# Kernel optimization log

Measured on AMD Instinct MI355X. Metric: run time of the kernel, lower is better.

## Reference

```python
import jax, jax.numpy as jnp
import numpy as np

N = 100000        # nodes
E = 1600000       # edges (before self-loops)
IN_CH = 256       # input features
HEADS = 8         # conv1 heads; per-head dim also 8 (GATConv(in, heads, heads=heads))
HID = 8
NCLASS = 64
SLOPE = 0.2       # PyG leaky_relu negative slope


def _gat_conv(x, edge_index, W, att_src, att_dst, bias, heads, ch, concat):
    """PyG GATConv (eval mode): gather -> leaky_relu score -> segment softmax -> scatter."""
    n = x.shape[0]
    src, dst = edge_index[0], edge_index[1]
    h = (x @ W).reshape(n, heads, ch)                      # [N, H, C]
    a_src = jnp.einsum('nhc,hc->nh', h, att_src)           # [N, H]
    a_dst = jnp.einsum('nhc,hc->nh', h, att_dst)
    alpha = jax.nn.leaky_relu(a_src[src] + a_dst[dst], SLOPE)  # [E, H]
    # segment softmax over destination node
    amax = jax.ops.segment_max(alpha, dst, num_segments=n)     # [N, H]
    ex = jnp.exp(alpha - amax[dst])
    denom = jax.ops.segment_sum(ex, dst, num_segments=n)
    coef = ex / (denom[dst] + 1e-16)                           # [E, H]
    out = jax.ops.segment_sum(coef[:, :, None] * h[src], dst, num_segments=n)  # [N, H, C]
    if concat:
        out = out.reshape(n, heads * ch)
    else:
        out = out.mean(axis=1)
    return out + bias


def _add_self_loops(edge_index, n):
    loop = jnp.arange(n, dtype=edge_index.dtype)
    return jnp.concatenate([edge_index, jnp.stack([loop, loop])], axis=1)


def setup_inputs() -> dict:
    key = jax.random.key(0)
    ks = jax.random.split(key, 10)
    g = lambda k, shp, s: (jax.random.normal(k, shp, jnp.float32) * s)
    return {
        'x': jax.random.normal(ks[0], (N, IN_CH), jnp.float32),
        'edge_index': jax.random.randint(ks[1], (2, E), 0, N, dtype=jnp.int64),
        'W1': g(ks[2], (IN_CH, HEADS * HID), 1.0 / np.sqrt(IN_CH)),
        'att_src1': g(ks[3], (HEADS, HID), 0.3),
        'att_dst1': g(ks[4], (HEADS, HID), 0.3),
        'b1': jnp.zeros((HEADS * HID,), jnp.float32),
        'W2': g(ks[5], (HEADS * HID, NCLASS), 1.0 / np.sqrt(HEADS * HID)),
        'att_src2': g(ks[6], (1, NCLASS), 0.3),
        'att_dst2': g(ks[7], (1, NCLASS), 0.3),
        'b2': jnp.zeros((NCLASS,), jnp.float32),
    }


def reference(x, edge_index, W1, att_src1, att_dst1, b1, W2, att_src2, att_dst2, b2):
    ei = _add_self_loops(edge_index, x.shape[0])
    h = jax.nn.elu(_gat_conv(x, ei, W1, att_src1, att_dst1, b1, HEADS, HID, True))
    # dropout is a no-op in eval mode
    h = _gat_conv(h, ei, W2, att_src2, att_dst2, b2, 1, NCLASS, False)
    return jax.nn.log_softmax(h, axis=-1)
```

## Files before the change

kernel.cpp:

```cpp
#include <hip/hip_runtime.h>
#include <hip/hip_bf16.h>

#define LRELU_SLOPE 0.2f
#define NBUK 256
#define BCAP 9728
#define CH2 6144

typedef unsigned int uint;
typedef unsigned short ushort;
typedef short bt8 __attribute__((ext_vector_type(8)));
typedef float fx4 __attribute__((ext_vector_type(4)));

__device__ __forceinline__ ushort f2bf(float f) {
    uint u = __float_as_uint(f);
    return (ushort)((u + 0x7FFF + ((u >> 16) & 1)) >> 16);
}
__device__ __forceinline__ float bf2f(ushort h) {
    return __uint_as_float(((uint)h) << 16);
}

#define ACC8(e, hv) \
    acc[0] += (e) * bf2f((ushort)((hv).x & 0xffff)); \
    acc[1] += (e) * bf2f((ushort)((hv).x >> 16));    \
    acc[2] += (e) * bf2f((ushort)((hv).y & 0xffff)); \
    acc[3] += (e) * bf2f((ushort)((hv).y >> 16));    \
    acc[4] += (e) * bf2f((ushort)((hv).z & 0xffff)); \
    acc[5] += (e) * bf2f((ushort)((hv).z >> 16));    \
    acc[6] += (e) * bf2f((ushort)((hv).w & 0xffff)); \
    acc[7] += (e) * bf2f((ushort)((hv).w >> 16));

__global__ __launch_bounds__(256) void prep_init(
    const float* __restrict__ W1, const float* __restrict__ W2,
    ushort* __restrict__ WT1, ushort* __restrict__ WT2, int* __restrict__ pcur)
{
    int t = threadIdx.x;
    int idx = blockIdx.x * 256 + t;
    if (blockIdx.x == 0) pcur[t] = t * BCAP;
    if (idx < 64 * 256) {
        int c = idx >> 8, k = idx & 255;
        WT1[idx] = f2bf(W1[k * 64 + c]);
    }
    int i2 = idx - 64 * 256;
    if (i2 >= 0 && i2 < 64 * 64) {
        int c = i2 >> 6, k = i2 & 63;
        WT2[i2] = f2bf(W2[k * 64 + c]);
    }
}

__global__ __launch_bounds__(1024) void partition_pairs(
    const int* __restrict__ ei, int E_, int ET,
    int* __restrict__ pcur, uint* __restrict__ pairs)
{
    __shared__ int lcnt[NBUK], lsc[NBUK], lplace[NBUK], gpos[NBUK];
    const int t = threadIdx.x;
    const int base = blockIdx.x * CH2;
    const int total = min(CH2, ET - base);
    if (total <= 0) return;

    if (t < NBUK) lcnt[t] = 0;
    __syncthreads();

    uint pp[6]; int pk[6];
    #pragma unroll
    for (int i = 0; i < 6; ++i) {
        int idx = t + i * 1024;
        pk[i] = -1;
        if (idx < total) {
            int e = base + idx;
            int s, d;
            if (e < E_) { s = ei[e]; d = ei[E_ + e]; } else { s = d = e - E_; }
            pk[i] = d >> 9;
            pp[i] = (uint)s | ((uint)(d & 511) << 17);
            atomicAdd(&lcnt[pk[i]], 1);
        }
    }
    __syncthreads();

    if (t < NBUK) lsc[t] = lcnt[t];
    __syncthreads();
    for (int off = 1; off < NBUK; off <<= 1) {
        int add = 0;
        if (t < NBUK && t >= off) add = lsc[t - off];
        __syncthreads();
        if (t < NBUK) lsc[t] += add;
        __syncthreads();
    }
    if (t < NBUK) {
        int excl = lsc[t] - lcnt[t];
        lplace[t] = excl;
        int c = lcnt[t];
        gpos[t] = c ? (atomicAdd(&pcur[t], c) - excl) : 0;
    }
    __syncthreads();

    #pragma unroll
    for (int i = 0; i < 6; ++i) {
        if (pk[i] >= 0) {
            int slot = atomicAdd(&lplace[pk[i]], 1);
            pairs[gpos[pk[i]] + slot] = pp[i];
        }
    }
}

__global__ __launch_bounds__(1024) void phase2_build(
    const uint* __restrict__ pairs, const int* __restrict__ pcur,
    int* __restrict__ rp, int* __restrict__ ssrc, int n, int nbuk_used)
{
    __shared__ int hist[512], cur[512], psc[NBUK];
    const int k = blockIdx.x;
    const int t = threadIdx.x;
    const int beg = k * BCAP;
    const int cnt = pcur[k] - beg;
    const int dbase = k << 9;

    if (t < 512) hist[t] = 0;
    if (t < NBUK) psc[t] = (t < nbuk_used) ? (pcur[t] - t * BCAP) : 0;
    __syncthreads();
    for (int off = 1; off < NBUK; off <<= 1) {
        int add = (t < NBUK && t >= off) ? psc[t - off] : 0;
        __syncthreads();
        if (t < NBUK) psc[t] += add;
        __syncthreads();
    }
    const int bbase = k ? psc[k - 1] : 0;

    for (int i = t; i < cnt; i += 1024)
        atomicAdd(&hist[pairs[beg + i] >> 17], 1);
    __syncthreads();

    int c0 = (t < 512) ? hist[t] : 0;
    for (int off = 1; off < 512; off <<= 1) {
        int add = (t < 512 && t >= off) ? hist[t - off] : 0;
        __syncthreads();
        if (t < 512) hist[t] += add;
        __syncthreads();
    }
    if (t < 512) {
        int node = dbase + t;
        if (node < n) rp[node] = bbase + hist[t];
        cur[t] = hist[t] - c0;
    }
    __syncthreads();

    for (int i = t; i < cnt; i += 1024) {
        uint p = pairs[beg + i];
        int j = p >> 17;
        int pos = bbase + atomicAdd(&cur[j], 1);
        ssrc[pos] = (int)(p & 0x1FFFF);
    }
}

template<int K, bool INF32, int HEADS>
__global__ __launch_bounds__(256) void gemm_att(
    const void* __restrict__ Xv, const ushort* __restrict__ WT,
    ushort* __restrict__ OUT, float* __restrict__ a_src, float* __restrict__ a_dst,
    const float* __restrict__ att_s, const float* __restrict__ att_d, int nrows)
{
    constexpr int LDW = K + 8;
    constexpr int NIT = K / 32;
    __shared__ ushort wt_l[64 * LDW];
    __shared__ ushort a_l[64 * 40];
    const int t = threadIdx.x;
    const int base = blockIdx.x * 64;

    for (int idx = t * 8; idx < 64 * K; idx += 256 * 8) {
        int r = idx / K, c = idx % K;
        *(uint4*)&wt_l[r * LDW + c] = *(const uint4*)&WT[idx];
    }

    const int w = t >> 6, l = t & 63;
    const int frow = l & 15;
    const int kof = (l >> 4) * 8;
    fx4 acc[4] = {};

    float4 rv0, rv1;
    uint4  rb;

    auto load_tile = [&](int k0) {
        if constexpr (INF32) {
            const float* X = (const float*)Xv;
            int kq = (t & 7) * 4;
            int r0 = (t >> 3), r1 = r0 + 32;
            int g0 = base + r0, g1 = base + r1;
            rv0 = make_float4(0.f, 0.f, 0.f, 0.f);
            rv1 = make_float4(0.f, 0.f, 0.f, 0.f);
            if (g0 < nrows) rv0 = *(const float4*)(X + (size_t)g0 * K + k0 + kq);
            if (g1 < nrows) rv1 = *(const float4*)(X + (size_t)g1 * K + k0 + kq);
        } else {
            const ushort* X = (const ushort*)Xv;
            int r = t >> 2, kq = (t & 3) * 8;
            int gr = base + r;
            rb = make_uint4(0, 0, 0, 0);
            if (gr < nrows) rb = *(const uint4*)(X + (size_t)gr * K + k0 + kq);
        }
    };
    auto store_tile = [&]() {
        if constexpr (INF32) {
            int kq = (t & 7) * 4;
            int r0 = (t >> 3);
            ushort4 o0, o1;
            o0.x = f2bf(rv0.x); o0.y = f2bf(rv0.y); o0.z = f2bf(rv0.z); o0.w = f2bf(rv0.w);
            o1.x = f2bf(rv1.x); o1.y = f2bf(rv1.y); o1.z = f2bf(rv1.z); o1.w = f2bf(rv1.w);
            *(ushort4*)&a_l[r0 * 40 + kq] = o0;
            *(ushort4*)&a_l[(r0 + 32) * 40 + kq] = o1;
        } else {
            int r = t >> 2, kq = (t & 3) * 8;
            *(uint4*)&a_l[r * 40 + kq] = rb;
        }
    };

    load_tile(0);
    store_tile();
    for (int it = 0; it < NIT; ++it) {
        if (it + 1 < NIT) load_tile((it + 1) * 32);
        __syncthreads();
        bt8 af = *(const bt8*)&a_l[(16 * w + frow) * 40 + kof];
        #pragma unroll
        for (int g = 0; g < 4; ++g) {
            bt8 bf = *(const bt8*)&wt_l[(16 * g + frow) * LDW + it * 32 + kof];
            acc[g] = __builtin_amdgcn_mfma_f32_16x16x32_bf16(af, bf, acc[g], 0, 0, 0);
        }
        __syncthreads();
        if (it + 1 < NIT) store_tile();
    }

    const int orow0 = base + 16 * w + (l >> 4) * 4;
    const int ocol = l & 15;
    #pragma unroll
    for (int g = 0; g < 4; ++g) {
        #pragma unroll
        for (int r4 = 0; r4 < 4; ++r4) {
            int gr = orow0 + r4;
            if (gr < nrows) OUT[(size_t)gr * 64 + 16 * g + ocol] = f2bf(acc[g][r4]);
        }
    }

    float as_c[4], ad_c[4];
    #pragma unroll
    for (int g = 0; g < 4; ++g) {
        as_c[g] = att_s[16 * g + ocol];
        ad_c[g] = att_d[16 * g + ocol];
    }
    if constexpr (HEADS == 8) {
        #pragma unroll
        for (int r4 = 0; r4 < 4; ++r4) {
            int gr = orow0 + r4;
            #pragma unroll
            for (int g = 0; g < 4; ++g) {
                float ps = acc[g][r4] * as_c[g];
                float pd = acc[g][r4] * ad_c[g];
                ps += __shfl_xor(ps, 1, 64); pd += __shfl_xor(pd, 1, 64);
                ps += __shfl_xor(ps, 2, 64); pd += __shfl_xor(pd, 2, 64);
                ps += __shfl_xor(ps, 4, 64); pd += __shfl_xor(pd, 4, 64);
                if ((l & 7) == 0 && gr < nrows) {
                    int head = 2 * g + ((l >> 3) & 1);
                    a_src[(size_t)gr * 8 + head] = ps;
                    a_dst[(size_t)gr * 8 + head] = pd;
                }
            }
        }
    } else {
        #pragma unroll
        for (int r4 = 0; r4 < 4; ++r4) {
            int gr = orow0 + r4;
            float ps = 0.f, pd = 0.f;
            #pragma unroll
            for (int g = 0; g < 4; ++g) {
                ps += acc[g][r4] * as_c[g];
                pd += acc[g][r4] * ad_c[g];
            }
            ps += __shfl_xor(ps, 1, 64); pd += __shfl_xor(pd, 1, 64);
            ps += __shfl_xor(ps, 2, 64); pd += __shfl_xor(pd, 2, 64);
            ps += __shfl_xor(ps, 4, 64); pd += __shfl_xor(pd, 4, 64);
            ps += __shfl_xor(ps, 8, 64); pd += __shfl_xor(pd, 8, 64);
            if ((l & 15) == 0 && gr < nrows) {
                a_src[gr] = ps;
                a_dst[gr] = pd;
            }
        }
    }
}

__global__ __launch_bounds__(256) void gather_h8(
    const int* __restrict__ rp, const int* __restrict__ ssrc,
    const float* __restrict__ a_src, const float* __restrict__ a_dst,
    const ushort* __restrict__ HB, const float* __restrict__ bias,
    ushort* __restrict__ HACT, int n)
{
    int node = blockIdx.x * 32 + (threadIdx.x >> 3);
    if (node >= n) return;
    int ol = threadIdx.x & 7;
    int end = rp[node];
    int start = node ? rp[node - 1] : 0;
    float adh = a_dst[(size_t)node * 8 + ol];
    float acc[8] = {};
    float dsum = 0.f;

    int i0 = start;
    for (; i0 + 16 <= end; i0 += 16) {
        int svA = ssrc[i0 + ol];
        int svB = ssrc[i0 + 8 + ol];
        #pragma unroll
        for (int j = 0; j < 8; ++j) {
            int sjA = __shfl(svA, j, 8);
            float aA = a_src[(size_t)sjA * 8 + ol] + adh;
            aA = aA > 0.f ? aA : LRELU_SLOPE * aA;
            float eA = __expf(aA);
            uint4 hvA = *(const uint4*)(HB + (size_t)sjA * 64 + ol * 8);
            dsum += eA; ACC8(eA, hvA);
            int sjB = __shfl(svB, j, 8);
            float aB = a_src[(size_t)sjB * 8 + ol] + adh;
            aB = aB > 0.f ? aB : LRELU_SLOPE * aB;
            float eB = __expf(aB);
            uint4 hvB = *(const uint4*)(HB + (size_t)sjB * 64 + ol * 8);
            dsum += eB; ACC8(eB, hvB);
        }
    }
    for (; i0 < end; i0 += 8) {
        int cnt = min(8, end - i0);
        int sv = (ol < cnt) ? ssrc[i0 + ol] : 0;
        #pragma unroll
        for (int j = 0; j < 8; ++j) {
            int sj = __shfl(sv, j, 8);
            float a = a_src[(size_t)sj * 8 + ol] + adh;
            a = a > 0.f ? a : LRELU_SLOPE * a;
            float e = __expf(a);
            e = (j < cnt) ? e : 0.f;
            uint4 hv = *(const uint4*)(HB + (size_t)sj * 64 + ol * 8);
            dsum += e; ACC8(e, hv);
        }
    }
    float inv = 1.f / (dsum + 1e-16f);
    float4 b0 = *(const float4*)(bias + ol * 8);
    float4 b1 = *(const float4*)(bias + ol * 8 + 4);
    float v[8];
    v[0] = acc[0] * inv + b0.x; v[1] = acc[1] * inv + b0.y;
    v[2] = acc[2] * inv + b0.z; v[3] = acc[3] * inv + b0.w;
    v[4] = acc[4] * inv + b1.x; v[5] = acc[5] * inv + b1.y;
    v[6] = acc[6] * inv + b1.z; v[7] = acc[7] * inv + b1.w;
    #pragma unroll
    for (int c = 0; c < 8; ++c) v[c] = v[c] > 0.f ? v[c] : expm1f(v[c]);
    uint4 o;
    o.x = (uint)f2bf(v[0]) | ((uint)f2bf(v[1]) << 16);
    o.y = (uint)f2bf(v[2]) | ((uint)f2bf(v[3]) << 16);
    o.z = (uint)f2bf(v[4]) | ((uint)f2bf(v[5]) << 16);
    o.w = (uint)f2bf(v[6]) | ((uint)f2bf(v[7]) << 16);
    *(uint4*)(HACT + (size_t)node * 64 + ol * 8) = o;
}

__global__ __launch_bounds__(256) void gather_h1_lsm(
    const int* __restrict__ rp, const int* __restrict__ ssrc,
    const float* __restrict__ a_src, const float* __restrict__ a_dst,
    const ushort* __restrict__ HB, const float* __restrict__ bias,
    float* __restrict__ OUT, int n)
{
    int node = blockIdx.x * 32 + (threadIdx.x >> 3);
    if (node >= n) return;
    int ol = threadIdx.x & 7;
    int end = rp[node];
    int start = node ? rp[node - 1] : 0;
    float ad = a_dst[node];
    float acc[8] = {};
    float dsum = 0.f;

    int i0 = start;
    for (; i0 + 16 <= end; i0 += 16) {
        int svA = ssrc[i0 + ol];
        int svB = ssrc[i0 + 8 + ol];
        #pragma unroll
        for (int j = 0; j < 8; ++j) {
            int sjA = __shfl(svA, j, 8);
            float aA = a_src[sjA] + ad;
            aA = aA > 0.f ? aA : LRELU_SLOPE * aA;
            float eA = __expf(aA);
            uint4 hvA = *(const uint4*)(HB + (size_t)sjA * 64 + ol * 8);
            dsum += eA; ACC8(eA, hvA);
            int sjB = __shfl(svB, j, 8);
            float aB = a_src[sjB] + ad;
            aB = aB > 0.f ? aB : LRELU_SLOPE * aB;
            float eB = __expf(aB);
            uint4 hvB = *(const uint4*)(HB + (size_t)sjB * 64 + ol * 8);
            dsum += eB; ACC8(eB, hvB);
        }
    }
    for (; i0 < end; i0 += 8) {
        int cnt = min(8, end - i0);
        int sv = (ol < cnt) ? ssrc[i0 + ol] : 0;
        #pragma unroll
        for (int j = 0; j < 8; ++j) {
            int sj = __shfl(sv, j, 8);
            float a = a_src[sj] + ad;
            a = a > 0.f ? a : LRELU_SLOPE * a;
            float e = __expf(a);
            e = (j < cnt) ? e : 0.f;
            uint4 hv = *(const uint4*)(HB + (size_t)sj * 64 + ol * 8);
            dsum += e; ACC8(e, hv);
        }
    }
    float inv = 1.f / (dsum + 1e-16f);
    float4 b0 = *(const float4*)(bias + ol * 8);
    float4 b1 = *(const float4*)(bias + ol * 8 + 4);
    float v[8];
    v[0] = acc[0] * inv + b0.x; v[1] = acc[1] * inv + b0.y;
    v[2] = acc[2] * inv + b0.z; v[3] = acc[3] * inv + b0.w;
    v[4] = acc[4] * inv + b1.x; v[5] = acc[5] * inv + b1.y;
    v[6] = acc[6] * inv + b1.z; v[7] = acc[7] * inv + b1.w;

    float m = v[0];
    #pragma unroll
    for (int c = 1; c < 8; ++c) m = fmaxf(m, v[c]);
    m = fmaxf(m, __shfl_xor(m, 1, 8));
    m = fmaxf(m, __shfl_xor(m, 2, 8));
    m = fmaxf(m, __shfl_xor(m, 4, 8));
    float s = 0.f;
    #pragma unroll
    for (int c = 0; c < 8; ++c) s += __expf(v[c] - m);
    s += __shfl_xor(s, 1, 8);
    s += __shfl_xor(s, 2, 8);
    s += __shfl_xor(s, 4, 8);
    float lse = m + __logf(s);
    float4 o0 = make_float4(v[0] - lse, v[1] - lse, v[2] - lse, v[3] - lse);
    float4 o1 = make_float4(v[4] - lse, v[5] - lse, v[6] - lse, v[7] - lse);
    *(float4*)(OUT + (size_t)node * 64 + ol * 8) = o0;
    *(float4*)(OUT + (size_t)node * 64 + ol * 8 + 4) = o1;
}

extern "C" void kernel_launch(void* const* d_in, const int* in_sizes, int n_in,
                              void* d_out, int out_size, void* d_ws, size_t ws_size,
                              hipStream_t stream)
{
    const float* x    = (const float*)d_in[0];
    const int*   ei   = (const int*)d_in[1];
    const float* W1   = (const float*)d_in[2];
    const float* as1w = (const float*)d_in[3];
    const float* ad1w = (const float*)d_in[4];
    const float* b1   = (const float*)d_in[5];
    const float* W2   = (const float*)d_in[6];
    const float* as2w = (const float*)d_in[7];
    const float* ad2w = (const float*)d_in[8];
    const float* b2   = (const float*)d_in[9];
    float* out = (float*)d_out;

    const int n  = in_sizes[0] / 256;
    const int E_ = in_sizes[1] / 2;
    const int ET = E_ + n;
    const int NBUKU = (n + 511) >> 9;

    char* wsb = (char*)d_ws;
    uint*   pairs= (uint*)wsb;
    ushort* HB   = (ushort*)(pairs + (size_t)NBUK*BCAP);
    ushort* HACT = HB + (size_t)n * 64;
    float*  a_s1 = (float*)(HACT + (size_t)n * 64);
    float*  a_d1 = a_s1 + (size_t)n * 8;
    float*  a_s2 = a_d1 + (size_t)n * 8;
    float*  a_d2 = a_s2 + n;
    int*    rp   = (int*)(a_d2 + n);
    int*    pcur = rp + n;
    int*    ssrc = pcur + NBUK;
    ushort* WT1  = (ushort*)(ssrc + ET);
    ushort* WT2  = WT1 + 64 * 256;

    const int gemm_grid = (n + 63) / 64;
    const int gath_grid = (n + 31) / 32;
    const int part_grid = (ET + CH2 - 1) / CH2;

    prep_init<<<80, 256, 0, stream>>>(W1, W2, WT1, WT2, pcur);
    partition_pairs<<<part_grid, 1024, 0, stream>>>(ei, E_, ET, pcur, pairs);
    phase2_build<<<NBUKU, 1024, 0, stream>>>(pairs, pcur, rp, ssrc, n, NBUKU);
    gemm_att<256, true, 8><<<gemm_grid, 256, 0, stream>>>(
        x, WT1, HB, a_s1, a_d1, as1w, ad1w, n);
    gather_h8<<<gath_grid, 256, 0, stream>>>(rp, ssrc, a_s1, a_d1, HB, b1, HACT, n);
    gemm_att<64, false, 1><<<gemm_grid, 256, 0, stream>>>(
        HACT, WT2, HB, a_s2, a_d2, as2w, ad2w, n);
    gather_h1_lsm<<<gath_grid, 256, 0, stream>>>(rp, ssrc, a_s2, a_d2, HB, b2, out, n);
}
```

Measured before the change: 190.0 us.

## Fuse edge partition and layer-1 GEMM into one heterogeneous kernel launch

```diff
diff --git a/kernel.cpp b/kernel.cpp
--- a/kernel.cpp
+++ b/kernel.cpp
@@ -47,13 +47,13 @@
     }
 }
 
-__global__ __launch_bounds__(1024) void partition_pairs(
-    const int* __restrict__ ei, int E_, int ET,
-    int* __restrict__ pcur, uint* __restrict__ pairs)
-{
-    __shared__ int lcnt[NBUK], lsc[NBUK], lplace[NBUK], gpos[NBUK];
+__device__ __forceinline__ void partition_body(
+    int bid, const int* __restrict__ ei, int E_, int ET,
+    int* __restrict__ pcur, uint* __restrict__ pairs,
+    int* lcnt, int* lsc, int* lplace, int* gpos)
+{
     const int t = threadIdx.x;
-    const int base = blockIdx.x * CH2;
+    const int base = bid * CH2;
     const int total = min(CH2, ET - base);
     if (total <= 0) return;
 
@@ -102,6 +102,115 @@
     }
 }
 
+__device__ __forceinline__ void gemm1_body4(
+    int gbid, const float* __restrict__ X, const ushort* __restrict__ WT,
+    ushort* __restrict__ OUT, float* __restrict__ a_src, float* __restrict__ a_dst,
+    const float* __restrict__ att_s, const float* __restrict__ att_d, int nrows,
+    ushort* wt_l, ushort* a_l)
+{
+    constexpr int K = 256, LDW = K + 8, NIT = K / 32;
+    const int t = threadIdx.x;
+    const int tt = t & 255;
+    const int base = (gbid * 4 + (t >> 8)) * 64;
+
+    for (int idx = t * 8; idx < 64 * K; idx += 1024 * 8) {
+        int r = idx / K, c = idx % K;
+        *(uint4*)&wt_l[r * LDW + c] = *(const uint4*)&WT[idx];
+    }
+
+    const int w = tt >> 6, l = tt & 63;
+    const int frow = l & 15;
+    const int kof = (l >> 4) * 8;
+    fx4 acc[4] = {};
+    float4 rv0, rv1;
+
+    auto load_tile = [&](int k0) {
+        int kq = (tt & 7) * 4;
+        int r0 = (tt >> 3);
+        int g0 = base + r0, g1 = base + r0 + 32;
+        rv0 = make_float4(0.f, 0.f, 0.f, 0.f);
+        rv1 = make_float4(0.f, 0.f, 0.f, 0.f);
+        if (g0 < nrows) rv0 = *(const float4*)(X + (size_t)g0 * K + k0 + kq);
+        if (g1 < nrows) rv1 = *(const float4*)(X + (size_t)g1 * K + k0 + kq);
+    };
+    auto store_tile = [&]() {
+        int kq = (tt & 7) * 4;
+        int r0 = (tt >> 3);
+        ushort4 o0, o1;
+        o0.x = f2bf(rv0.x); o0.y = f2bf(rv0.y); o0.z = f2bf(rv0.z); o0.w = f2bf(rv0.w);
+        o1.x = f2bf(rv1.x); o1.y = f2bf(rv1.y); o1.z = f2bf(rv1.z); o1.w = f2bf(rv1.w);
+        *(ushort4*)&a_l[r0 * 40 + kq] = o0;
+        *(ushort4*)&a_l[(r0 + 32) * 40 + kq] = o1;
+    };
+
+    load_tile(0);
+    store_tile();
+    for (int it = 0; it < NIT; ++it) {
+        if (it + 1 < NIT) load_tile((it + 1) * 32);
+        __syncthreads();
+        bt8 af = *(const bt8*)&a_l[(16 * w + frow) * 40 + kof];
+        #pragma unroll
+        for (int g = 0; g < 4; ++g) {
+            bt8 bf = *(const bt8*)&wt_l[(16 * g + frow) * LDW + it * 32 + kof];
+            acc[g] = __builtin_amdgcn_mfma_f32_16x16x32_bf16(af, bf, acc[g], 0, 0, 0);
+        }
+        __syncthreads();
+        if (it + 1 < NIT) store_tile();
+    }
+
+    const int orow0 = base + 16 * w + (l >> 4) * 4;
+    const int ocol = l & 15;
+    #pragma unroll
+    for (int g = 0; g < 4; ++g) {
+        #pragma unroll
+        for (int r4 = 0; r4 < 4; ++r4) {
+            int gr = orow0 + r4;
+            if (gr < nrows) OUT[(size_t)gr * 64 + 16 * g + ocol] = f2bf(acc[g][r4]);
+        }
+    }
+
+    float as_c[4], ad_c[4];
+    #pragma unroll
+    for (int g = 0; g < 4; ++g) {
+        as_c[g] = att_s[16 * g + ocol];
+        ad_c[g] = att_d[16 * g + ocol];
+    }
+    #pragma unroll
+    for (int r4 = 0; r4 < 4; ++r4) {
+        int gr = orow0 + r4;
+        #pragma unroll
+        for (int g = 0; g < 4; ++g) {
+            float ps = acc[g][r4] * as_c[g];
+            float pd = acc[g][r4] * ad_c[g];
+            ps += __shfl_xor(ps, 1, 64); pd += __shfl_xor(pd, 1, 64);
+            ps += __shfl_xor(ps, 2, 64); pd += __shfl_xor(pd, 2, 64);
+            ps += __shfl_xor(ps, 4, 64); pd += __shfl_xor(pd, 4, 64);
+            if ((l & 7) == 0 && gr < nrows) {
+                int head = 2 * g + ((l >> 3) & 1);
+                a_src[(size_t)gr * 8 + head] = ps;
+                a_dst[(size_t)gr * 8 + head] = pd;
+            }
+        }
+    }
+}
+
+__global__ __launch_bounds__(1024) void part_gemm1(
+    const int* __restrict__ ei, int E_, int ET, int part_grid,
+    int* __restrict__ pcur, uint* __restrict__ pairs,
+    const float* __restrict__ x, const ushort* __restrict__ WT1,
+    ushort* __restrict__ HB, float* __restrict__ a_s1, float* __restrict__ a_d1,
+    const float* __restrict__ att_s, const float* __restrict__ att_d, int n)
+{
+    __shared__ int lcnt[NBUK], lsc[NBUK], lplace[NBUK], gpos[NBUK];
+    __shared__ ushort wt_l[64 * 264];
+    __shared__ ushort a_l4[4][64 * 40];
+    if ((int)blockIdx.x < part_grid)
+        partition_body(blockIdx.x, ei, E_, ET, pcur, pairs, lcnt, lsc, lplace, gpos);
+    else
+        gemm1_body4(blockIdx.x - part_grid, x, WT1, HB, a_s1, a_d1,
+                    att_s, att_d, n, wt_l, a_l4[threadIdx.x >> 8]);
+}
+
 __global__ __launch_bounds__(1024) void phase2_build(
     const uint* __restrict__ pairs, const int* __restrict__ pcur,
     int* __restrict__ rp, int* __restrict__ ssrc, int n, int nbuk_used)
@@ -150,14 +259,12 @@
     }
 }
 
-template<int K, bool INF32, int HEADS>
-__global__ __launch_bounds__(256) void gemm_att(
-    const void* __restrict__ Xv, const ushort* __restrict__ WT,
+__global__ __launch_bounds__(256) void gemm2_att(
+    const ushort* __restrict__ X, const ushort* __restrict__ WT,
     ushort* __restrict__ OUT, float* __restrict__ a_src, float* __restrict__ a_dst,
     const float* __restrict__ att_s, const float* __restrict__ att_d, int nrows)
 {
-    constexpr int LDW = K + 8;
-    constexpr int NIT = K / 32;
+    constexpr int K = 64, LDW = K + 8, NIT = K / 32;
     __shared__ ushort wt_l[64 * LDW];
     __shared__ ushort a_l[64 * 40];
     const int t = threadIdx.x;
@@ -172,41 +279,17 @@
     const int frow = l & 15;
     const int kof = (l >> 4) * 8;
     fx4 acc[4] = {};
-
-    float4 rv0, rv1;
-    uint4  rb;
+    uint4 rb;
 
     auto load_tile = [&](int k0) {
-        if constexpr (INF32) {
-            const float* X = (const float*)Xv;
-            int kq = (t & 7) * 4;
-            int r0 = (t >> 3), r1 = r0 + 32;
-            int g0 = base + r0, g1 = base + r1;
-            rv0 = make_float4(0.f, 0.f, 0.f, 0.f);
-            rv1 = make_float4(0.f, 0.f, 0.f, 0.f);
-            if (g0 < nrows) rv0 = *(const float4*)(X + (size_t)g0 * K + k0 + kq);
-            if (g1 < nrows) rv1 = *(const float4*)(X + (size_t)g1 * K + k0 + kq);
-        } else {
-            const ushort* X = (const ushort*)Xv;
-            int r = t >> 2, kq = (t & 3) * 8;
-            int gr = base + r;
-            rb = make_uint4(0, 0, 0, 0);
-            if (gr < nrows) rb = *(const uint4*)(X + (size_t)gr * K + k0 + kq);
-        }
+        int r = t >> 2, kq = (t & 3) * 8;
+        int gr = base + r;
+        rb = make_uint4(0, 0, 0, 0);
+        if (gr < nrows) rb = *(const uint4*)(X + (size_t)gr * K + k0 + kq);
     };
     auto store_tile = [&]() {
-        if constexpr (INF32) {
-            int kq = (t & 7) * 4;
-            int r0 = (t >> 3);
-            ushort4 o0, o1;
-            o0.x = f2bf(rv0.x); o0.y = f2bf(rv0.y); o0.z = f2bf(rv0.z); o0.w = f2bf(rv0.w);
-            o1.x = f2bf(rv1.x); o1.y = f2bf(rv1.y); o1.z = f2bf(rv1.z); o1.w = f2bf(rv1.w);
-            *(ushort4*)&a_l[r0 * 40 + kq] = o0;
-            *(ushort4*)&a_l[(r0 + 32) * 40 + kq] = o1;
-        } else {
-            int r = t >> 2, kq = (t & 3) * 8;
-            *(uint4*)&a_l[r * 40 + kq] = rb;
-        }
+        int r = t >> 2, kq = (t & 3) * 8;
+        *(uint4*)&a_l[r * 40 + kq] = rb;
     };
 
     load_tile(0);
@@ -241,42 +324,22 @@
         as_c[g] = att_s[16 * g + ocol];
         ad_c[g] = att_d[16 * g + ocol];
     }
-    if constexpr (HEADS == 8) {
-        #pragma unroll
-        for (int r4 = 0; r4 < 4; ++r4) {
-            int gr = orow0 + r4;
-            #pragma unroll
-            for (int g = 0; g < 4; ++g) {
-                float ps = acc[g][r4] * as_c[g];
-                float pd = acc[g][r4] * ad_c[g];
-                ps += __shfl_xor(ps, 1, 64); pd += __shfl_xor(pd, 1, 64);
-                ps += __shfl_xor(ps, 2, 64); pd += __shfl_xor(pd, 2, 64);
-                ps += __shfl_xor(ps, 4, 64); pd += __shfl_xor(pd, 4, 64);
-                if ((l & 7) == 0 && gr < nrows) {
-                    int head = 2 * g + ((l >> 3) & 1);
-                    a_src[(size_t)gr * 8 + head] = ps;
-                    a_dst[(size_t)gr * 8 + head] = pd;
-                }
-            }
-        }
-    } else {
-        #pragma unroll
-        for (int r4 = 0; r4 < 4; ++r4) {
-            int gr = orow0 + r4;
-            float ps = 0.f, pd = 0.f;
-            #pragma unroll
-            for (int g = 0; g < 4; ++g) {
-                ps += acc[g][r4] * as_c[g];
-                pd += acc[g][r4] * ad_c[g];
-            }
-            ps += __shfl_xor(ps, 1, 64); pd += __shfl_xor(pd, 1, 64);
-            ps += __shfl_xor(ps, 2, 64); pd += __shfl_xor(pd, 2, 64);
-            ps += __shfl_xor(ps, 4, 64); pd += __shfl_xor(pd, 4, 64);
-            ps += __shfl_xor(ps, 8, 64); pd += __shfl_xor(pd, 8, 64);
-            if ((l & 15) == 0 && gr < nrows) {
-                a_src[gr] = ps;
-                a_dst[gr] = pd;
-            }
+    #pragma unroll
+    for (int r4 = 0; r4 < 4; ++r4) {
+        int gr = orow0 + r4;
+        float ps = 0.f, pd = 0.f;
+        #pragma unroll
+        for (int g = 0; g < 4; ++g) {
+            ps += acc[g][r4] * as_c[g];
+            pd += acc[g][r4] * ad_c[g];
+        }
+        ps += __shfl_xor(ps, 1, 64); pd += __shfl_xor(pd, 1, 64);
+        ps += __shfl_xor(ps, 2, 64); pd += __shfl_xor(pd, 2, 64);
+        ps += __shfl_xor(ps, 4, 64); pd += __shfl_xor(pd, 4, 64);
+        ps += __shfl_xor(ps, 8, 64); pd += __shfl_xor(pd, 8, 64);
+        if ((l & 15) == 0 && gr < nrows) {
+            a_src[gr] = ps;
+            a_dst[gr] = pd;
         }
     }
 }
@@ -460,17 +523,16 @@
     ushort* WT1  = (ushort*)(ssrc + ET);
     ushort* WT2  = WT1 + 64 * 256;
 
-    const int gemm_grid = (n + 63) / 64;
-    const int gath_grid = (n + 31) / 32;
-    const int part_grid = (ET + CH2 - 1) / CH2;
+    const int gemm_grid  = (n + 63) / 64;
+    const int gemm_grid4 = (n + 255) / 256;
+    const int gath_grid  = (n + 31) / 32;
+    const int part_grid  = (ET + CH2 - 1) / CH2;
 
     prep_init<<<80, 256, 0, stream>>>(W1, W2, WT1, WT2, pcur);
-    partition_pairs<<<part_grid, 1024, 0, stream>>>(ei, E_, ET, pcur, pairs);
+    part_gemm1<<<part_grid + gemm_grid4, 1024, 0, stream>>>(
+        ei, E_, ET, part_grid, pcur, pairs, x, WT1, HB, a_s1, a_d1, as1w, ad1w, n);
     phase2_build<<<NBUKU, 1024, 0, stream>>>(pairs, pcur, rp, ssrc, n, NBUKU);
-    gemm_att<256, true, 8><<<gemm_grid, 256, 0, stream>>>(
-        x, WT1, HB, a_s1, a_d1, as1w, ad1w, n);
     gather_h8<<<gath_grid, 256, 0, stream>>>(rp, ssrc, a_s1, a_d1, HB, b1, HACT, n);
-    gemm_att<64, false, 1><<<gemm_grid, 256, 0, stream>>>(
-        HACT, WT2, HB, a_s2, a_d2, as2w, ad2w, n);
+    gemm2_att<<<gemm_grid, 256, 0, stream>>>(HACT, WT2, HB, a_s2, a_d2, as2w, ad2w, n);
     gather_h1_lsm<<<gath_grid, 256, 0, stream>>>(rp, ssrc, a_s2, a_d2, HB, b2, out, n);
 }
```

After: 179.3 us. -5.6%, faster.
